# Kernel tuning notes

Measured on AMD Instinct MI355X. Metric: run time of the kernel, lower is better.

Reference implementation:

```python
import jax, jax.numpy as jnp
import numpy as np

N = 50000
E = 800000
F_IN = 128
HID = 16
HEADS = 8
CLS = 16
NEG_SLOPE = 0.2


def setup_inputs() -> dict:
    key = jax.random.key(0)
    ks = jax.random.split(key, 12)
    x = jax.random.normal(ks[0], (N, F_IN), dtype=jnp.float32)
    edge_index = jax.random.randint(ks[1], (2, E), 0, N, dtype=jnp.int32)
    s = 0.1
    W1 = jax.random.normal(ks[2], (F_IN, HEADS * HID), dtype=jnp.float32) * s
    att_src1 = jax.random.normal(ks[3], (HEADS, HID), dtype=jnp.float32) * s
    att_dst1 = jax.random.normal(ks[4], (HEADS, HID), dtype=jnp.float32) * s
    b1 = jax.random.normal(ks[5], (HEADS * HID,), dtype=jnp.float32) * s
    W2 = jax.random.normal(ks[6], (HEADS * HID, CLS), dtype=jnp.float32) * s
    att_src2 = jax.random.normal(ks[7], (1, CLS), dtype=jnp.float32) * s
    att_dst2 = jax.random.normal(ks[8], (1, CLS), dtype=jnp.float32) * s
    b2 = jax.random.normal(ks[9], (CLS,), dtype=jnp.float32) * s
    return {"x": x, "edge_index": edge_index, "W1": W1, "att_src1": att_src1,
            "att_dst1": att_dst1, "b1": b1, "W2": W2, "att_src2": att_src2,
            "att_dst2": att_dst2, "b2": b2}


def _gat_conv(x, src, dst, W, a_src, a_dst, b, heads, out_ch, concat):
    n = x.shape[0]
    h = (x @ W).reshape(n, heads, out_ch)                     # [N,H,C]
    alpha_src = (h * a_src[None]).sum(-1)                     # [N,H]
    alpha_dst = (h * a_dst[None]).sum(-1)                     # [N,H]
    e = jax.nn.leaky_relu(alpha_src[src] + alpha_dst[dst], NEG_SLOPE)  # [E,H]
    m = jax.lax.stop_gradient(jax.ops.segment_max(e, dst, num_segments=n))
    e = jnp.exp(e - m[dst])
    denom = jax.ops.segment_sum(e, dst, num_segments=n)
    alpha = e / (denom[dst] + 1e-16)                          # [E,H]
    msg = h[src] * alpha[:, :, None]                          # [E,H,C]
    out = jax.ops.segment_sum(msg, dst, num_segments=n)       # [N,H,C]
    out = out.reshape(n, heads * out_ch) if concat else out.mean(axis=1)
    return out + b


def reference(x, edge_index, W1, att_src1, att_dst1, b1, W2, att_src2, att_dst2, b2):
    # PyG GATConv default add_self_loops=True
    loop = jnp.arange(N, dtype=edge_index.dtype)
    src = jnp.concatenate([edge_index[0], loop])
    dst = jnp.concatenate([edge_index[1], loop])
    h = _gat_conv(x, src, dst, W1, att_src1, att_dst1, b1, HEADS, HID, True)
    h = jax.nn.elu(h)
    # dropout inactive (eval mode)
    out = _gat_conv(h, src, dst, W2, att_src2, att_dst2, b2, 1, CLS, False)
    return out
```

## Files before the change

### kernel.cpp

```cpp
#include <hip/hip_runtime.h>
#include <hip/hip_bf16.h>
#include <limits.h>
#include <math.h>

#define N 50000
#define E_ 800000
#define ETOT 850000
#define HH 128
#define HEADS 8
#define HID 16
#define CLS 16
#define NEG 0.2f
#define NB ((N + 255) / 256)
#define GBM 64
#define GEMM_NB ((N + GBM - 1) / GBM)
#define LINK_NB ((ETOT + 255) / 256)
#define PREP_NB ((128*128 + 255) / 256)
#define A1_NB ((N*HEADS + 255) / 256)

typedef unsigned short u16;
typedef unsigned int   u32;
typedef unsigned long long u64;
typedef short s8v __attribute__((ext_vector_type(8)));
typedef float f4v __attribute__((ext_vector_type(4)));

__device__ __forceinline__ u16 f2bu(float f){
  union{float f; u32 i;} c; c.f = f;
  u32 lsb = (c.i >> 16) & 1u;
  c.i += 0x7fffu + lsb;
  return (u16)(c.i >> 16);
}
__device__ __forceinline__ float bu2f(u16 u){
  union{u32 i; float f;} c; c.i = ((u32)u) << 16; return c.f;
}
__device__ __forceinline__ float blo(u32 u){ union{u32 i; float f;} c; c.i = u << 16; return c.f; }
__device__ __forceinline__ float bhi(u32 u){ union{u32 i; float f;} c; c.i = u & 0xffff0000u; return c.f; }

__global__ __launch_bounds__(256) void k_init(int* __restrict__ head){
  int i = blockIdx.x*256 + threadIdx.x;
  if(i < N) head[i] = -1;
}

__global__ __launch_bounds__(256) void k_linkprep(const int* __restrict__ ei,
                                                  int* __restrict__ head,
                                                  u64* __restrict__ nsrc,
                                                  const float* __restrict__ W1,
                                                  const float* __restrict__ W2,
                                                  u16* __restrict__ wth, u16* __restrict__ wtl,
                                                  u16* __restrict__ w2th, u16* __restrict__ w2tl){
  if(blockIdx.x < PREP_NB){
    int i = blockIdx.x*256 + threadIdx.x;
    if(i < 128*128){
      int k = i >> 7, c = i & 127;
      float v = W1[i];
      u16 hi = f2bu(v);
      wth[c*128 + k] = hi;
      wtl[c*128 + k] = f2bu(v - bu2f(hi));
    }
    if(i < 128*16){
      int k = i >> 4, c = i & 15;
      float v = W2[i];
      u16 hi = f2bu(v);
      w2th[c*128 + k] = hi;
      w2tl[c*128 + k] = f2bu(v - bu2f(hi));
    }
    return;
  }
  int e = (blockIdx.x - PREP_NB)*256 + threadIdx.x;
  if(e >= ETOT) return;
  int s, d;
  if(e < E_){ s = ei[e]; d = ei[E_ + e]; } else { s = d = e - E_; }
  int old = atomicExch(&head[d], e);
  nsrc[e] = ((u64)(u32)s << 32) | (u32)old;
}

__global__ __launch_bounds__(256) void k_gemm1walk(const float* __restrict__ x,
                                                   const u16* __restrict__ wth,
                                                   const u16* __restrict__ wtl,
                                                   u16* __restrict__ h1b,
                                                   const int* __restrict__ head,
                                                   const u64* __restrict__ nsrc,
                                                   int* __restrict__ deg,
                                                   int* __restrict__ bsum){
  __shared__ u16 xh[GBM][40], xl[GBM][40];
  __shared__ u16 wh[128][40], wl[128][40];
  __shared__ int sm[256];
  if(blockIdx.x >= GEMM_NB){
    int b = blockIdx.x - GEMM_NB;
    int t = threadIdx.x;
    int i = b*256 + t;
    int cnt = 0;
    if(i < N){
      int e = head[i];
      while(e >= 0){ cnt++; e = (int)(u32)(nsrc[e] & 0xffffffffu); }
      deg[i] = cnt;
    }
    sm[t] = cnt;
    __syncthreads();
    #pragma unroll
    for(int ofs=128; ofs>0; ofs>>=1){
      if(t < ofs) sm[t] += sm[t+ofs];
      __syncthreads();
    }
    if(t == 0) bsum[b] = sm[0];
    return;
  }
  int tid  = threadIdx.x;
  int wv   = tid >> 6;
  int lane = tid & 63;
  int row0 = blockIdx.x * GBM;

  f4v acc[4][2];
  #pragma unroll
  for(int t=0;t<4;t++)
    #pragma unroll
    for(int u=0;u<2;u++) acc[t][u] = (f4v){0.f,0.f,0.f,0.f};

  int xr  = tid >> 2;
  int xkq = (tid & 3) * 8;
  int wc  = tid & 127;
  int wq  = (tid >> 7) * 8;
  int xrow = row0 + xr; if(xrow >= N) xrow = N-1;
  const float* xb = x + (size_t)xrow*128 + xkq;
  int fr = lane & 15, fg = lane >> 4;
  int kk = fg*8;

  for(int kc=0; kc<4; kc++){
    int k0 = kc*32;
    float4 v0 = *(const float4*)(xb + k0);
    float4 v1 = *(const float4*)(xb + k0 + 4);
    __syncthreads();
    {
      float vv[8] = {v0.x,v0.y,v0.z,v0.w,v1.x,v1.y,v1.z,v1.w};
      s8v H, L;
      #pragma unroll
      for(int j=0;j<8;j++){
        u16 h_ = f2bu(vv[j]);
        H[j] = (short)h_;
        L[j] = (short)f2bu(vv[j] - bu2f(h_));
      }
      *(s8v*)&xh[xr][xkq] = H;
      *(s8v*)&xl[xr][xkq] = L;
    }
    #pragma unroll
    for(int j=0;j<2;j++){
      int kq = wq + j*16;
      *(s8v*)&wh[wc][kq] = *(const s8v*)&wth[wc*128 + k0 + kq];
      *(s8v*)&wl[wc][kq] = *(const s8v*)&wtl[wc*128 + k0 + kq];
    }
    __syncthreads();
    s8v a_h[4], a_l[4], b_h[2], b_l[2];
    #pragma unroll
    for(int t=0;t<4;t++){
      a_h[t] = *(const s8v*)&xh[t*16 + fr][kk];
      a_l[t] = *(const s8v*)&xl[t*16 + fr][kk];
    }
    #pragma unroll
    for(int u=0;u<2;u++){
      int col = wv*32 + u*16 + fr;
      b_h[u] = *(const s8v*)&wh[col][kk];
      b_l[u] = *(const s8v*)&wl[col][kk];
    }
    #pragma unroll
    for(int t=0;t<4;t++){
      #pragma unroll
      for(int u=0;u<2;u++){
        acc[t][u] = __builtin_amdgcn_mfma_f32_16x16x32_bf16(a_h[t], b_h[u], acc[t][u], 0,0,0);
        acc[t][u] = __builtin_amdgcn_mfma_f32_16x16x32_bf16(a_h[t], b_l[u], acc[t][u], 0,0,0);
        acc[t][u] = __builtin_amdgcn_mfma_f32_16x16x32_bf16(a_l[t], b_h[u], acc[t][u], 0,0,0);
      }
    }
  }
  #pragma unroll
  for(int t=0;t<4;t++){
    #pragma unroll
    for(int j=0;j<4;j++){
      int row = row0 + t*16 + fg*4 + j;
      if(row < N){
        u16* dst = h1b + (size_t)row*128 + wv*32 + fr;
        dst[0]  = f2bu(acc[t][0][j]);
        dst[16] = f2bu(acc[t][1][j]);
      }
    }
  }
}

__global__ __launch_bounds__(256) void k_scan3alpha(const int* __restrict__ deg,
                                                    const int* __restrict__ bsum,
                                                    const int* __restrict__ head,
                                                    const u64* __restrict__ nsrc,
                                                    int* __restrict__ off,
                                                    int* __restrict__ csr,
                                                    const u16* __restrict__ h1b,
                                                    const float* __restrict__ Asv,
                                                    const float* __restrict__ Adv,
                                                    float* __restrict__ as1,
                                                    float* __restrict__ ad1){
  __shared__ int red[256];
  __shared__ int sm[256];
  if(blockIdx.x < NB){
    int t = threadIdx.x;
    red[t] = (t < blockIdx.x) ? bsum[t] : 0;
    __syncthreads();
    #pragma unroll
    for(int ofs=128; ofs>0; ofs>>=1){
      if(t < ofs) red[t] += red[t+ofs];
      __syncthreads();
    }
    int boff = red[0];
    int i = blockIdx.x*256 + t;
    int v0 = (i < N) ? deg[i] : 0;
    sm[t] = v0;
    __syncthreads();
    #pragma unroll
    for(int ofs=1; ofs<256; ofs<<=1){
      int v = sm[t];
      int add = (t >= ofs) ? sm[t-ofs] : 0;
      __syncthreads();
      sm[t] = v + add;
      __syncthreads();
    }
    if(i < N){
      int excl = boff + sm[t] - v0;
      off[i] = excl;
      if(i == N-1) off[N] = excl + v0;
      int e = head[i];
      int pos = excl;
      while(e >= 0){
        u64 v = nsrc[e];
        csr[pos++] = (int)(v >> 32);
        e = (int)(u32)(v & 0xffffffffu);
      }
    }
    return;
  }
  int id = (blockIdx.x - NB)*256 + threadIdx.x;
  if(id >= N*HEADS) return;
  int i = id >> 3, h = id & 7;
  const uint4* hv = (const uint4*)(h1b + (size_t)i*HH + h*HID);
  uint4 u0 = hv[0], u1 = hv[1];
  float vals[16] = {blo(u0.x),bhi(u0.x),blo(u0.y),bhi(u0.y),
                    blo(u0.z),bhi(u0.z),blo(u0.w),bhi(u0.w),
                    blo(u1.x),bhi(u1.x),blo(u1.y),bhi(u1.y),
                    blo(u1.z),bhi(u1.z),blo(u1.w),bhi(u1.w)};
  float s=0.f, d=0.f;
  #pragma unroll
  for(int j=0;j<16;j++){
    s = fmaf(vals[j], Asv[h*HID+j], s);
    d = fmaf(vals[j], Adv[h*HID+j], d);
  }
  as1[id]=s; ad1[id]=d;
}

#define CH 32
__global__ __launch_bounds__(256) void k_agg1(const int* __restrict__ off,
                                              const int* __restrict__ csr,
                                              const float* __restrict__ as1,
                                              const float* __restrict__ ad1,
                                              const u32* __restrict__ h1w,
                                              const float* __restrict__ b1,
                                              u32* __restrict__ helu_w){
  __shared__ float wsm[4][CH*8];
  __shared__ int   ssm[4][CH];
  int wv   = threadIdx.x >> 6;
  int lane = threadIdx.x & 63;
  int node = blockIdx.x*4 + wv;
  int beg = off[node], end = off[node+1];
  int h  = lane >> 3;
  int hh = lane & 7;
  int el = lane >> 3;
  float advA = ad1[node*8 + hh];
  float den = 0.f, num0 = 0.f, num1 = 0.f;
  float* wsw = wsm[wv];
  int*   ssw = ssm[wv];
  const u32* hp = h1w + lane;
  for(int base = beg; base < end; base += CH){
    int cnt = end - base; if(cnt > CH) cnt = CH;
    #pragma unroll
    for(int k=0;k<CH;k+=8){
      int e = el + k;
      if(e < cnt){
        int s = csr[base+e];
        if(hh == 0) ssw[e] = s;
        float v = as1[s*8+hh] + advA;
        v = v > 0.f ? v : NEG*v;
        wsw[e*8+hh] = __expf(v);
      }
    }
    int e = 0;
    for(; e+8 <= cnt; e += 8){
      int ss[8]; float ww[8]; u32 uu[8];
      #pragma unroll
      for(int j=0;j<8;j++){ ss[j] = ssw[e+j]; ww[j] = wsw[(e+j)*8+h]; }
      #pragma unroll
      for(int j=0;j<8;j++){ uu[j] = hp[(size_t)ss[j]*64]; }
      #pragma unroll
      for(int j=0;j<8;j++){
        den += ww[j];
        num0 = fmaf(ww[j], blo(uu[j]), num0);
        num1 = fmaf(ww[j], bhi(uu[j]), num1);
      }
    }
    for(; e+4 <= cnt; e += 4){
      int ss[4]; float ww[4]; u32 uu[4];
      #pragma unroll
      for(int j=0;j<4;j++){ ss[j] = ssw[e+j]; ww[j] = wsw[(e+j)*8+h]; }
      #pragma unroll
      for(int j=0;j<4;j++){ uu[j] = hp[(size_t)ss[j]*64]; }
      #pragma unroll
      for(int j=0;j<4;j++){
        den += ww[j];
        num0 = fmaf(ww[j], blo(uu[j]), num0);
        num1 = fmaf(ww[j], bhi(uu[j]), num1);
      }
    }
    for(; e < cnt; e++){
      int s = ssw[e];
      float w = wsw[e*8+h];
      u32 u = hp[(size_t)s*64];
      den += w;
      num0 = fmaf(w, blo(u), num0);
      num1 = fmaf(w, bhi(u), num1);
    }
  }
  float2 bb = ((const float2*)b1)[lane];
  float inv = 1.f / (den + 1e-16f);
  float r0 = num0*inv + bb.x;
  float r1 = num1*inv + bb.y;
  r0 = r0 > 0.f ? r0 : expm1f(r0);
  r1 = r1 > 0.f ? r1 : expm1f(r1);
  helu_w[(size_t)node*64 + lane] = (u32)f2bu(r0) | ((u32)f2bu(r1) << 16);
}

__global__ __launch_bounds__(256) void k_gemm2m(const u16* __restrict__ helu,
                                                const u16* __restrict__ w2th,
                                                const u16* __restrict__ w2tl,
                                                const float* __restrict__ Asv,
                                                const float* __restrict__ Adv,
                                                u16* __restrict__ h2b,
                                                float* __restrict__ as2,
                                                float* __restrict__ ad2){
  __shared__ u16 At[4][16][136];
  __shared__ u16 Bh[16][136], Bl[16][136];
  int tid  = threadIdx.x;
  int wv   = tid >> 6;
  int lane = tid & 63;
  int fr = lane & 15, fg = lane >> 4;
  int row0 = blockIdx.x*64 + wv*16;

  {
    int r = tid >> 4, c8 = (tid & 15)*8;
    *(s8v*)&Bh[r][c8] = *(const s8v*)&w2th[r*128 + c8];
    *(s8v*)&Bl[r][c8] = *(const s8v*)&w2tl[r*128 + c8];
  }
  #pragma unroll
  for(int j=0;j<4;j++){
    int rl = j*4 + (lane >> 4);
    int rg = row0 + rl; if(rg >= N) rg = N-1;
    *(s8v*)&At[wv][rl][(lane & 15)*8] = *(const s8v*)&helu[(size_t)rg*128 + (lane & 15)*8];
  }
  __syncthreads();

  f4v acc = (f4v){0.f,0.f,0.f,0.f};
  #pragma unroll
  for(int kc=0; kc<4; kc++){
    int kk = kc*32 + fg*8;
    s8v a  = *(const s8v*)&At[wv][fr][kk];
    s8v bh = *(const s8v*)&Bh[fr][kk];
    s8v bl = *(const s8v*)&Bl[fr][kk];
    acc = __builtin_amdgcn_mfma_f32_16x16x32_bf16(a, bh, acc, 0,0,0);
    acc = __builtin_amdgcn_mfma_f32_16x16x32_bf16(a, bl, acc, 0,0,0);
  }
  float asv = Asv[fr], adv = Adv[fr];
  #pragma unroll
  for(int j=0;j<4;j++){
    int row = row0 + fg*4 + j;
    float ps = acc[j]*asv, pd = acc[j]*adv;
    ps += __shfl_xor(ps,1); ps += __shfl_xor(ps,2); ps += __shfl_xor(ps,4); ps += __shfl_xor(ps,8);
    pd += __shfl_xor(pd,1); pd += __shfl_xor(pd,2); pd += __shfl_xor(pd,4); pd += __shfl_xor(pd,8);
    if(row < N){
      h2b[(size_t)row*16 + fr] = f2bu(acc[j]);
      if(fr == 0){ as2[row] = ps; ad2[row] = pd; }
    }
  }
}

__global__ __launch_bounds__(256) void k_agg2(const int* __restrict__ off,
                                              const int* __restrict__ csr,
                                              const float* __restrict__ as2,
                                              const float* __restrict__ ad2,
                                              const u32* __restrict__ h2w,
                                              const float* __restrict__ b2,
                                              float* __restrict__ outp){
  int t = threadIdx.x;
  int node = blockIdx.x*32 + (t >> 3);
  int c2 = t & 7;
  if(node >= N) return;
  int beg = off[node], end = off[node+1];
  float adv = ad2[node];
  float den = 0.f, num0 = 0.f, num1 = 0.f;
  int gbase = t & 56;
  for(int base = beg; base < end; base += 8){
    int cnt = end - base; if(cnt > 8) cnt = 8;
    float w_my = 0.f; int s_my = 0;
    if(c2 < cnt){
      s_my = csr[base + c2];
      float v = as2[s_my] + adv;
      v = v > 0.f ? v : NEG*v;
      w_my = __expf(v);
    }
    float ww[8]; int ss[8]; u32 uu[8];
    #pragma unroll
    for(int j=0;j<8;j++){
      ww[j] = __shfl(w_my, gbase | j);
      ss[j] = __shfl(s_my, gbase | j);
    }
    #pragma unroll
    for(int j=0;j<8;j++){
      if(j < cnt) uu[j] = h2w[(size_t)ss[j]*8 + c2];
    }
    #pragma unroll
    for(int j=0;j<8;j++){
      if(j < cnt){
        den += ww[j];
        num0 = fmaf(ww[j], blo(uu[j]), num0);
        num1 = fmaf(ww[j], bhi(uu[j]), num1);
      }
    }
  }
  float inv = 1.f / (den + 1e-16f);
  float2 bb = ((const float2*)b2)[c2];
  float2 r;
  r.x = num0*inv + bb.x;
  r.y = num1*inv + bb.y;
  ((float2*)outp)[(size_t)node*8 + c2] = r;
}

extern "C" void kernel_launch(void* const* d_in, const int* in_sizes, int n_in,
                              void* d_out, int out_size, void* d_ws, size_t ws_size,
                              hipStream_t stream){
  const float* x     = (const float*)d_in[0];
  const int*   ei    = (const int*)  d_in[1];
  const float* W1    = (const float*)d_in[2];
  const float* av_s1 = (const float*)d_in[3];
  const float* av_d1 = (const float*)d_in[4];
  const float* b1    = (const float*)d_in[5];
  const float* W2    = (const float*)d_in[6];
  const float* av_s2 = (const float*)d_in[7];
  const float* av_d2 = (const float*)d_in[8];
  const float* b2    = (const float*)d_in[9];
  float* outp = (float*)d_out;

  char* p = (char*)d_ws;
  auto alloc = [&](size_t bytes){ char* q = p; p += (bytes + 255) & ~(size_t)255; return q; };
  u16*   h1b    = (u16*)  alloc((size_t)N*HH*2);
  u16*   helu_b = (u16*)  alloc((size_t)N*HH*2);
  u16*   h2b    = (u16*)  alloc((size_t)N*CLS*2);
  float* as1    = (float*)alloc((size_t)N*HEADS*4);
  float* ad1    = (float*)alloc((size_t)N*HEADS*4);
  float* as2    = (float*)alloc((size_t)N*4);
  float* ad2    = (float*)alloc((size_t)N*4);
  int*   deg    = (int*)  alloc((size_t)N*4);
  int*   head   = (int*)  alloc((size_t)N*4);
  int*   off    = (int*)  alloc((size_t)(N+1)*4);
  int*   csr    = (int*)  alloc((size_t)ETOT*4);
  u64*   nsrc   = (u64*)  alloc((size_t)ETOT*8);
  u16*   wth    = (u16*)  alloc((size_t)128*128*2);
  u16*   wtl    = (u16*)  alloc((size_t)128*128*2);
  u16*   w2th   = (u16*)  alloc((size_t)16*128*2);
  u16*   w2tl   = (u16*)  alloc((size_t)16*128*2);
  int*   bsum   = (int*)  alloc((size_t)NB*4);

  k_init<<<NB, 256, 0, stream>>>(head);

  k_linkprep<<<PREP_NB + LINK_NB, 256, 0, stream>>>(ei, head, nsrc,
                                                    W1, W2, wth, wtl, w2th, w2tl);

  k_gemm1walk<<<GEMM_NB + NB, 256, 0, stream>>>(x, wth, wtl, h1b, head, nsrc, deg, bsum);

  k_scan3alpha<<<NB + A1_NB, 256, 0, stream>>>(deg, bsum, head, nsrc, off, csr,
                                               h1b, av_s1, av_d1, as1, ad1);

  k_agg1<<<N/4, 256, 0, stream>>>(off, csr, as1, ad1, (const u32*)h1b, b1, (u32*)helu_b);

  k_gemm2m<<<(N+63)/64, 256, 0, stream>>>(helu_b, w2th, w2tl, av_s2, av_d2, h2b, as2, ad2);
  k_agg2<<<(N+31)/32, 256, 0, stream>>>(off, csr, as2, ad2, (const u32*)h2b, b2, outp);
}
```

Measured before the change: 145.6 us.

## Fuse layer-2 projection GEMM into layer-1 aggregation epilogue

Each wavefront in k_agg1 now writes its ELU row into its shared scratch and right away runs a per-node MFMA against W2 (hi/lo bf16 split). It also computes the layer-2 attention logits in place. This removes the k_gemm2m launch and the full N×128 bf16 helu round trip through global memory. The cost is that each node's MFMA uses only one of its 16 rows, so 15/16 of that compute is wasted, and the W2 tiles are read from global (likely cached) per wave instead of being staged in LDS. The scratch reuse also depends on the aggregation loop having finished with wsw; there is no explicit wave barrier, but the data is wave-local.

```diff
diff --git a/kernel.cpp b/kernel.cpp
--- a/kernel.cpp
+++ b/kernel.cpp
@@ -259,7 +259,13 @@
                                               const float* __restrict__ ad1,
                                               const u32* __restrict__ h1w,
                                               const float* __restrict__ b1,
-                                              u32* __restrict__ helu_w){
+                                              const u16* __restrict__ w2th,
+                                              const u16* __restrict__ w2tl,
+                                              const float* __restrict__ Asv2,
+                                              const float* __restrict__ Adv2,
+                                              u16* __restrict__ h2b,
+                                              float* __restrict__ as2,
+                                              float* __restrict__ ad2){
   __shared__ float wsm[4][CH*8];
   __shared__ int   ssm[4][CH];
   int wv   = threadIdx.x >> 6;
@@ -329,60 +335,27 @@
   float r1 = num1*inv + bb.y;
   r0 = r0 > 0.f ? r0 : expm1f(r0);
   r1 = r1 > 0.f ? r1 : expm1f(r1);
-  helu_w[(size_t)node*64 + lane] = (u32)f2bu(r0) | ((u32)f2bu(r1) << 16);
-}
-
-__global__ __launch_bounds__(256) void k_gemm2m(const u16* __restrict__ helu,
-                                                const u16* __restrict__ w2th,
-                                                const u16* __restrict__ w2tl,
-                                                const float* __restrict__ Asv,
-                                                const float* __restrict__ Adv,
-                                                u16* __restrict__ h2b,
-                                                float* __restrict__ as2,
-                                                float* __restrict__ ad2){
-  __shared__ u16 At[4][16][136];
-  __shared__ u16 Bh[16][136], Bl[16][136];
-  int tid  = threadIdx.x;
-  int wv   = tid >> 6;
-  int lane = tid & 63;
-  int fr = lane & 15, fg = lane >> 4;
-  int row0 = blockIdx.x*64 + wv*16;
-
-  {
-    int r = tid >> 4, c8 = (tid & 15)*8;
-    *(s8v*)&Bh[r][c8] = *(const s8v*)&w2th[r*128 + c8];
-    *(s8v*)&Bl[r][c8] = *(const s8v*)&w2tl[r*128 + c8];
-  }
-  #pragma unroll
-  for(int j=0;j<4;j++){
-    int rl = j*4 + (lane >> 4);
-    int rg = row0 + rl; if(rg >= N) rg = N-1;
-    *(s8v*)&At[wv][rl][(lane & 15)*8] = *(const s8v*)&helu[(size_t)rg*128 + (lane & 15)*8];
-  }
-  __syncthreads();
-
-  f4v acc = (f4v){0.f,0.f,0.f,0.f};
+
+  ((u32*)wsw)[lane] = (u32)f2bu(r0) | ((u32)f2bu(r1) << 16);
+  const u16* hrow = (const u16*)wsw;
+  int kk8 = (lane >> 4) * 8;
+  int c   = lane & 15;
+  f4v acc2 = (f4v){0.f,0.f,0.f,0.f};
   #pragma unroll
   for(int kc=0; kc<4; kc++){
-    int kk = kc*32 + fg*8;
-    s8v a  = *(const s8v*)&At[wv][fr][kk];
-    s8v bh = *(const s8v*)&Bh[fr][kk];
-    s8v bl = *(const s8v*)&Bl[fr][kk];
-    acc = __builtin_amdgcn_mfma_f32_16x16x32_bf16(a, bh, acc, 0,0,0);
-    acc = __builtin_amdgcn_mfma_f32_16x16x32_bf16(a, bl, acc, 0,0,0);
-  }
-  float asv = Asv[fr], adv = Adv[fr];
-  #pragma unroll
-  for(int j=0;j<4;j++){
-    int row = row0 + fg*4 + j;
-    float ps = acc[j]*asv, pd = acc[j]*adv;
-    ps += __shfl_xor(ps,1); ps += __shfl_xor(ps,2); ps += __shfl_xor(ps,4); ps += __shfl_xor(ps,8);
-    pd += __shfl_xor(pd,1); pd += __shfl_xor(pd,2); pd += __shfl_xor(pd,4); pd += __shfl_xor(pd,8);
-    if(row < N){
-      h2b[(size_t)row*16 + fr] = f2bu(acc[j]);
-      if(fr == 0){ as2[row] = ps; ad2[row] = pd; }
-    }
-  }
+    s8v a  = *(const s8v*)&hrow[kc*32 + kk8];
+    s8v bh = *(const s8v*)&w2th[c*128 + kc*32 + kk8];
+    s8v bl = *(const s8v*)&w2tl[c*128 + kc*32 + kk8];
+    acc2 = __builtin_amdgcn_mfma_f32_16x16x32_bf16(a, bh, acc2, 0,0,0);
+    acc2 = __builtin_amdgcn_mfma_f32_16x16x32_bf16(a, bl, acc2, 0,0,0);
+  }
+  float h2v = acc2[0];
+  float ps = h2v * Asv2[c];
+  float pd = h2v * Adv2[c];
+  ps += __shfl_xor(ps,1); ps += __shfl_xor(ps,2); ps += __shfl_xor(ps,4); ps += __shfl_xor(ps,8);
+  pd += __shfl_xor(pd,1); pd += __shfl_xor(pd,2); pd += __shfl_xor(pd,4); pd += __shfl_xor(pd,8);
+  if(lane < 16) h2b[(size_t)node*16 + c] = f2bu(h2v);
+  if(lane == 0){ as2[node] = ps; ad2[node] = pd; }
 }
 
 __global__ __launch_bounds__(256) void k_agg2(const int* __restrict__ off,
@@ -454,7 +427,6 @@
   char* p = (char*)d_ws;
   auto alloc = [&](size_t bytes){ char* q = p; p += (bytes + 255) & ~(size_t)255; return q; };
   u16*   h1b    = (u16*)  alloc((size_t)N*HH*2);
-  u16*   helu_b = (u16*)  alloc((size_t)N*HH*2);
   u16*   h2b    = (u16*)  alloc((size_t)N*CLS*2);
   float* as1    = (float*)alloc((size_t)N*HEADS*4);
   float* ad1    = (float*)alloc((size_t)N*HEADS*4);
@@ -481,8 +453,8 @@
   k_scan3alpha<<<NB + A1_NB, 256, 0, stream>>>(deg, bsum, head, nsrc, off, csr,
                                                h1b, av_s1, av_d1, as1, ad1);
 
-  k_agg1<<<N/4, 256, 0, stream>>>(off, csr, as1, ad1, (const u32*)h1b, b1, (u32*)helu_b);
-
-  k_gemm2m<<<(N+63)/64, 256, 0, stream>>>(helu_b, w2th, w2tl, av_s2, av_d2, h2b, as2, ad2);
+  k_agg1<<<N/4, 256, 0, stream>>>(off, csr, as1, ad1, (const u32*)h1b, b1,
+                                  w2th, w2tl, av_s2, av_d2, h2b, as2, ad2);
+
   k_agg2<<<(N+31)/32, 256, 0, stream>>>(off, csr, as2, ad2, (const u32*)h2b, b2, outp);
 }
```

Measured after the change: 170.7 us. +17.2%, slower.
